# Performance work log

Measured on AMD Instinct MI355X. Metric: run time of the kernel, lower is better.

## Reference

```python
import jax, jax.numpy as jnp
import numpy as np


def _conv3x3(x, w, b):
    # standard 3x3 conv, stride 1, padding 1 (NCHW / OIHW)
    y = jax.lax.conv_general_dilated(x, w, window_strides=(1, 1),
                                     padding=((1, 1), (1, 1)),
                                     dimension_numbers=('NCHW', 'OIHW', 'NCHW'))
    return y + b[None, :, None, None]


def _bilinear_gather(img, py, px):
    # img [B,C,H,W]; py/px [B,K,H,W] fractional sample coords; zero outside (torchvision semantics)
    B, C, H, W = img.shape
    K = py.shape[1]
    y0f = jnp.floor(py)
    x0f = jnp.floor(px)
    dy = py - y0f
    dx = px - x0f
    y0 = y0f.astype(jnp.int32)
    x0 = x0f.astype(jnp.int32)
    img_f = img.reshape(B, C, H * W)

    def corner(yy, xx, wgt):
        valid = (yy >= 0) & (yy < H) & (xx >= 0) & (xx < W)
        idx = (jnp.clip(yy, 0, H - 1) * W + jnp.clip(xx, 0, W - 1)).reshape(B, -1)
        g = jax.vmap(lambda im, ix: im[:, ix])(img_f, idx)  # [B, C, K*H*W]
        return g * (wgt * valid).reshape(B, 1, -1)

    out = (corner(y0, x0, (1 - dy) * (1 - dx)) + corner(y0, x0 + 1, (1 - dy) * dx)
           + corner(y0 + 1, x0, dy * (1 - dx)) + corner(y0 + 1, x0 + 1, dy * dx))
    return out.reshape(B, C, K, H, W)


def _deform_conv(x, offset, w, b):
    # torchvision DeformConv2d, kernel 3, stride 1, pad 1, no groups
    # offset [B, 2*K, H, W], channel pairs (2k, 2k+1) = (dy, dx) for tap k
    B, C, H, W = x.shape
    K = 9
    off = offset.reshape(B, K, 2, H, W)
    ki, kj = jnp.meshgrid(jnp.arange(3), jnp.arange(3), indexing='ij')
    ki = (ki.reshape(K) - 1).astype(x.dtype)
    kj = (kj.reshape(K) - 1).astype(x.dtype)
    py = jnp.arange(H, dtype=x.dtype)[None, None, :, None] + ki[None, :, None, None] + off[:, :, 0]
    px = jnp.arange(W, dtype=x.dtype)[None, None, None, :] + kj[None, :, None, None] + off[:, :, 1]
    patches = _bilinear_gather(x, py, px)  # [B, C, K, H, W]
    out = jnp.einsum('bckhw,ock->bohw', patches, w.reshape(w.shape[0], C, K))
    return out + b[None, :, None, None]


def _maxpool2(x):
    return jax.lax.reduce_window(x, -jnp.inf, jax.lax.max, (1, 1, 2, 2), (1, 1, 2, 2), 'VALID')


def _forward(x, w_off1, b_off1, w1, b1, w_off2, b_off2, w2, b2,
             w_off3, b_off3, w3, b3, w_fc, b_fc):
    off = _conv3x3(x, w_off1, b_off1)
    h = jax.nn.relu(_deform_conv(x, off, w1, b1))
    h = _maxpool2(h)                       # [B,16,48,48]
    off = _conv3x3(h, w_off2, b_off2)
    h = jax.nn.relu(_deform_conv(h, off, w2, b2))
    h = _maxpool2(h)                       # [B,32,24,24]
    off = _conv3x3(h, w_off3, b_off3)
    h = jax.nn.relu(_deform_conv(h, off, w3, b3))  # [B,64,24,24]
    B, C, H, W = h.shape
    # adaptive avg pool to (3,3): 24 -> 3 exact bins of 8
    h = h.reshape(B, C, 3, H // 3, 3, W // 3).mean(axis=(3, 5))
    h = h.reshape(B, -1)                   # [B, 576]
    return h @ w_fc.T + b_fc


def setup_inputs() -> dict:
    key = jax.random.key(0)
    ks = jax.random.split(key, 16)
    f32 = jnp.float32

    def rn(k, shape, scale):
        return jax.random.normal(k, shape, dtype=f32) * scale

    return {
        'x': rn(ks[0], (64, 1, 96, 96), 1.0),
        # offset convs: small weights so offsets start near zero (standard deform init)
        'w_off1': rn(ks[1], (18, 1, 3, 3), 0.01), 'b_off1': jnp.zeros((18,), f32),
        'w1': rn(ks[2], (16, 1, 3, 3), 1.0 / 3.0), 'b1': jnp.zeros((16,), f32),
        'w_off2': rn(ks[3], (18, 16, 3, 3), 0.01), 'b_off2': jnp.zeros((18,), f32),
        'w2': rn(ks[4], (32, 16, 3, 3), 1.0 / 12.0), 'b2': jnp.zeros((32,), f32),
        'w_off3': rn(ks[5], (18, 32, 3, 3), 0.01), 'b_off3': jnp.zeros((18,), f32),
        'w3': rn(ks[6], (64, 32, 3, 3), 1.0 / 17.0), 'b3': jnp.zeros((64,), f32),
        'w_fc': rn(ks[7], (10, 576), 1.0 / 24.0), 'b_fc': jnp.zeros((10,), f32),
    }


def reference(x, w_off1, b_off1, w1, b1, w_off2, b_off2, w2, b2,
              w_off3, b_off3, w3, b3, w_fc, b_fc):
    return _forward(x, w_off1, b_off1, w1, b1, w_off2, b_off2, w2, b2,
                    w_off3, b_off3, w3, b3, w_fc, b_fc)
```

## Files before the change

kernel.cpp:

```cpp
#include <hip/hip_runtime.h>
#include <math.h>


template <int CIN, int COUT>
__global__ void wtrans(const float* __restrict__ w, float* __restrict__ wT) {
  int t = blockIdx.x * 256 + threadIdx.x;
  if (t >= 9 * CIN * COUT) return;
  int k = t / (CIN * COUT);
  int r = t % (CIN * COUT);
  int c = r / COUT;
  int o = r % COUT;
  wT[t] = w[(o * CIN + c) * 9 + k];
}

__global__ void deform1_fused(const float* __restrict__ x,
                              const float* __restrict__ woff,
                              const float* __restrict__ boff,
                              const float* __restrict__ w1,
                              const float* __restrict__ b1,
                              float* __restrict__ out) {
  const int H = 96, W = 96, HW = H * W;
  __shared__ float wos[9 * 18];
  __shared__ __align__(16) float ws1[9 * 16];
  for (int t = threadIdx.x; t < 9 * 18; t += 256) { int k = t / 18, tc = t % 18; wos[t] = woff[tc * 9 + k]; }
  for (int t = threadIdx.x; t < 9 * 16; t += 256) { int k = t / 16, o = t % 16; ws1[t] = w1[o * 9 + k]; }
  __syncthreads();

  int gid = blockIdx.x * 256 + threadIdx.x;
  int p2 = gid % (HW / 2);
  int b  = gid / (HW / 2);
  int xi0 = (2 * p2) % W, yi = (2 * p2) / W;
  const float* xb = x + (size_t)b * HW;

  float v[3][4];
#pragma unroll
  for (int r = 0; r < 3; ++r) {
    int yy = yi + r - 1;
    float my = (yy >= 0 && yy < H) ? 1.f : 0.f;
    int cy = min(max(yy, 0), H - 1);
#pragma unroll
    for (int c = 0; c < 4; ++c) {
      int xx = xi0 + c - 1;
      float mx = (xx >= 0 && xx < W) ? 1.f : 0.f;
      int cx = min(max(xx, 0), W - 1);
      v[r][c] = xb[cy * W + cx] * (my * mx);
    }
  }

  float off0[18], off1[18];
#pragma unroll
  for (int tc = 0; tc < 18; ++tc) { float bb = boff[tc]; off0[tc] = bb; off1[tc] = bb; }
#pragma unroll
  for (int r = 0; r < 3; ++r)
#pragma unroll
    for (int c = 0; c < 3; ++c) {
      float t0 = v[r][c], t1 = v[r][c + 1];
      const float2* wv = (const float2*)&wos[(r * 3 + c) * 18];
#pragma unroll
      for (int tt = 0; tt < 9; ++tt) {
        float2 ww = wv[tt];
        off0[2 * tt]     = fmaf(ww.x, t0, off0[2 * tt]);
        off0[2 * tt + 1] = fmaf(ww.y, t0, off0[2 * tt + 1]);
        off1[2 * tt]     = fmaf(ww.x, t1, off1[2 * tt]);
        off1[2 * tt + 1] = fmaf(ww.y, t1, off1[2 * tt + 1]);
      }
    }

  float acc0[16], acc1[16];
#pragma unroll
  for (int o = 0; o < 16; ++o) { float bb = b1[o]; acc0[o] = bb; acc1[o] = bb; }

#pragma unroll
  for (int k = 0; k < 9; ++k) {
    int dky = k / 3 - 1, dkx = k % 3 - 1;
    float val0, val1;
    {
      float py = (float)(yi + dky) + off0[2 * k];
      float px = (float)(xi0 + dkx) + off0[2 * k + 1];
      float y0f = floorf(py), x0f = floorf(px);
      float fy = py - y0f, fx = px - x0f;
      int y0 = (int)y0f, x0 = (int)x0f, y1 = y0 + 1, x1 = x0 + 1;
      float vy0 = (y0 >= 0 && y0 < H) ? 1.f : 0.f;
      float vy1 = (y1 >= 0 && y1 < H) ? 1.f : 0.f;
      float vx0 = (x0 >= 0 && x0 < W) ? 1.f : 0.f;
      float vx1 = (x1 >= 0 && x1 < W) ? 1.f : 0.f;
      float w00 = (1.f - fy) * (1.f - fx) * vy0 * vx0;
      float w01 = (1.f - fy) * fx * vy0 * vx1;
      float w10 = fy * (1.f - fx) * vy1 * vx0;
      float w11 = fy * fx * vy1 * vx1;
      int cy0 = min(max(y0, 0), H - 1), cy1 = min(max(y1, 0), H - 1);
      int cx0 = min(max(x0, 0), W - 1), cx1 = min(max(x1, 0), W - 1);
      float a = xb[cy0 * W + cx0], bb = xb[cy0 * W + cx1];
      float c = xb[cy1 * W + cx0], d = xb[cy1 * W + cx1];
      val0 = w00 * a + w01 * bb + w10 * c + w11 * d;
    }
    {
      float py = (float)(yi + dky) + off1[2 * k];
      float px = (float)(xi0 + 1 + dkx) + off1[2 * k + 1];
      float y0f = floorf(py), x0f = floorf(px);
      float fy = py - y0f, fx = px - x0f;
      int y0 = (int)y0f, x0 = (int)x0f, y1 = y0 + 1, x1 = x0 + 1;
      float vy0 = (y0 >= 0 && y0 < H) ? 1.f : 0.f;
      float vy1 = (y1 >= 0 && y1 < H) ? 1.f : 0.f;
      float vx0 = (x0 >= 0 && x0 < W) ? 1.f : 0.f;
      float vx1 = (x1 >= 0 && x1 < W) ? 1.f : 0.f;
      float w00 = (1.f - fy) * (1.f - fx) * vy0 * vx0;
      float w01 = (1.f - fy) * fx * vy0 * vx1;
      float w10 = fy * (1.f - fx) * vy1 * vx0;
      float w11 = fy * fx * vy1 * vx1;
      int cy0 = min(max(y0, 0), H - 1), cy1 = min(max(y1, 0), H - 1);
      int cx0 = min(max(x0, 0), W - 1), cx1 = min(max(x1, 0), W - 1);
      float a = xb[cy0 * W + cx0], bb = xb[cy0 * W + cx1];
      float c = xb[cy1 * W + cx0], d = xb[cy1 * W + cx1];
      val1 = w00 * a + w01 * bb + w10 * c + w11 * d;
    }
    const float4* wv = (const float4*)&ws1[k * 16];
#pragma unroll
    for (int q = 0; q < 4; ++q) {
      float4 w4 = wv[q];
      acc0[4 * q + 0] = fmaf(w4.x, val0, acc0[4 * q + 0]);
      acc0[4 * q + 1] = fmaf(w4.y, val0, acc0[4 * q + 1]);
      acc0[4 * q + 2] = fmaf(w4.z, val0, acc0[4 * q + 2]);
      acc0[4 * q + 3] = fmaf(w4.w, val0, acc0[4 * q + 3]);
      acc1[4 * q + 0] = fmaf(w4.x, val1, acc1[4 * q + 0]);
      acc1[4 * q + 1] = fmaf(w4.y, val1, acc1[4 * q + 1]);
      acc1[4 * q + 2] = fmaf(w4.z, val1, acc1[4 * q + 2]);
      acc1[4 * q + 3] = fmaf(w4.w, val1, acc1[4 * q + 3]);
    }
  }

  float* op = out + (size_t)b * 16 * HW + (size_t)yi * W + xi0;
#pragma unroll
  for (int o = 0; o < 16; ++o) {
    float2 r = make_float2(fmaxf(acc0[o], 0.f), fmaxf(acc1[o], 0.f));
    *(float2*)(op + (size_t)o * HW) = r;
  }
}

template <int C, int HI>
__global__ void pool_nchw_to_nhwc(const float* __restrict__ in,
                                  float* __restrict__ out) {
  const int HO = HI / 2, C4 = C / 4;
  int gid = blockIdx.x * blockDim.x + threadIdx.x;
  if (gid >= 64 * HO * HO * C4) return;
  int c4 = gid % C4;
  int t = gid / C4;
  int x = t % HO; t /= HO;
  int y = t % HO;
  int b = t / HO;
  float4 r;
  float* rp = &r.x;
#pragma unroll
  for (int cc = 0; cc < 4; ++cc) {
    int c = c4 * 4 + cc;
    const float* p = in + ((size_t)(b * C + c) * HI + 2 * y) * HI + 2 * x;
    rp[cc] = fmaxf(fmaxf(p[0], p[1]), fmaxf(p[HI], p[HI + 1]));
  }
  *(float4*)(out + (((size_t)b * HO + y) * HO + x) * C + c4 * 4) = r;
}

template <int CIN, int COUT, int NSPLIT>
__global__ __launch_bounds__(256, 4)
void conv3x3_off(const float* __restrict__ in,
                 const float* __restrict__ w,
                 const float* __restrict__ bias,
                 float* __restrict__ out,
                 int B, int H, int W) {
  constexpr int OC = COUT / NSPLIT;
  __shared__ float ws[9 * CIN * OC];
  int obase = blockIdx.y * OC;
  for (int t = threadIdx.x; t < 9 * CIN * OC; t += 256) {
    int k = t / (CIN * OC); int r = t % (CIN * OC);
    int c = r / OC; int o = r % OC;
    ws[t] = w[((obase + o) * CIN + c) * 9 + k];
  }
  __syncthreads();

  int gid = blockIdx.x * 256 + threadIdx.x;
  if (gid >= B * H * W) return;
  int x = gid % W; int t0 = gid / W; int y = t0 % H; int b = t0 / H;
  int HW = H * W;
  const float* inb = in + (size_t)b * HW * CIN;

  float acc[OC];
#pragma unroll
  for (int o = 0; o < OC; ++o) acc[o] = bias[obase + o];

#pragma unroll
  for (int ky = 0; ky < 3; ++ky) {
    int yy = y + ky - 1;
    if (yy < 0 || yy >= H) continue;
#pragma unroll
    for (int kx = 0; kx < 3; ++kx) {
      int xx = x + kx - 1;
      if (xx < 0 || xx >= W) continue;
      const float4* p4 = (const float4*)(inb + ((size_t)yy * W + xx) * CIN);
      int k = ky * 3 + kx;
#pragma unroll
      for (int c4 = 0; c4 < CIN / 4; ++c4) {
        float4 p = p4[c4];
        const float* pv = &p.x;
#pragma unroll
        for (int cc = 0; cc < 4; ++cc) {
          const float* wrow = &ws[(k * CIN + 4 * c4 + cc) * OC];
#pragma unroll
          for (int o = 0; o < OC; ++o) acc[o] = fmaf(wrow[o], pv[cc], acc[o]);
        }
      }
    }
  }

  float* op = out + (size_t)gid * 20 + obase;
#pragma unroll
  for (int o = 0; o < OC; ++o) op[o] = acc[o];
}

template <int CIN, int COUT, int HW_>
__global__ void deform_sgpr(const float* __restrict__ in,
                            const float* __restrict__ off_in,
                            const float* __restrict__ wT,
                            const float* __restrict__ bias,
                            float* __restrict__ out) {
  constexpr int H = HW_, W = HW_, HW = H * W;
  constexpr int PX = 64;
  constexpr int QT = CIN / 4;
  constexpr int QPT = QT / 4;
  constexpr int PSTR = 9 * CIN + 4;
  constexpr int OPG = COUT / 4;

  __shared__ __align__(16) float offs[PX * 20];
  __shared__ __align__(16) float patch[PX * PSTR];

  const int pixbase = blockIdx.x * PX;
  const int b = pixbase / HW;
  const int p0 = pixbase - b * HW;
  const float* inb = in + (size_t)b * HW * CIN;

  {
    const float4* src = (const float4*)(off_in + (size_t)pixbase * 20);
    for (int t = threadIdx.x; t < PX * 20 / 4; t += 256)
      ((float4*)offs)[t] = src[t];
  }
  __syncthreads();

  {
    int px = threadIdx.x & 63;
    int qp = threadIdx.x >> 6;
    int pib = p0 + px;
    int yi = pib / W, xi = pib % W;
#pragma unroll
    for (int k = 0; k < 9; ++k) {
      float py  = (float)(yi + k / 3 - 1) + offs[px * 20 + 2 * k];
      float pxx = (float)(xi + k % 3 - 1) + offs[px * 20 + 2 * k + 1];
      float y0f = floorf(py), x0f = floorf(pxx);
      float fy = py - y0f, fx = pxx - x0f;
      int y0 = (int)y0f, x0 = (int)x0f, y1 = y0 + 1, x1 = x0 + 1;
      float vy0 = (y0 >= 0 && y0 < H) ? 1.f : 0.f;
      float vy1 = (y1 >= 0 && y1 < H) ? 1.f : 0.f;
      float vx0 = (x0 >= 0 && x0 < W) ? 1.f : 0.f;
      float vx1 = (x1 >= 0 && x1 < W) ? 1.f : 0.f;
      float w00 = (1.f - fy) * (1.f - fx) * vy0 * vx0;
      float w01 = (1.f - fy) * fx * vy0 * vx1;
      float w10 = fy * (1.f - fx) * vy1 * vx0;
      float w11 = fy * fx * vy1 * vx1;
      int cy0 = min(max(y0, 0), H - 1), cy1 = min(max(y1, 0), H - 1);
      int cx0 = min(max(x0, 0), W - 1), cx1 = min(max(x1, 0), W - 1);
      const float* r00 = inb + ((size_t)cy0 * W + cx0) * CIN;
      const float* r01 = inb + ((size_t)cy0 * W + cx1) * CIN;
      const float* r10 = inb + ((size_t)cy1 * W + cx0) * CIN;
      const float* r11 = inb + ((size_t)cy1 * W + cx1) * CIN;
#pragma unroll
      for (int j = 0; j < QPT; ++j) {
        int q = qp + j * 4;
        float4 A  = *(const float4*)(r00 + 4 * q);
        float4 Bv = *(const float4*)(r01 + 4 * q);
        float4 Cv = *(const float4*)(r10 + 4 * q);
        float4 Dv = *(const float4*)(r11 + 4 * q);
        float4 val;
        val.x = w00 * A.x + w01 * Bv.x + w10 * Cv.x + w11 * Dv.x;
        val.y = w00 * A.y + w01 * Bv.y + w10 * Cv.y + w11 * Dv.y;
        val.z = w00 * A.z + w01 * Bv.z + w10 * Cv.z + w11 * Dv.z;
        val.w = w00 * A.w + w01 * Bv.w + w10 * Cv.w + w11 * Dv.w;
        *(float4*)&patch[px * PSTR + k * CIN + 4 * q] = val;
      }
    }
  }
  __syncthreads();

  int px = threadIdx.x & 63;
  int og = __builtin_amdgcn_readfirstlane(threadIdx.x >> 6);
  int obase = og * OPG;

  float acc[OPG];
#pragma unroll
  for (int o = 0; o < OPG; ++o) acc[o] = bias[obase + o];

  const float* patp = &patch[px * PSTR];
  for (int k = 0; k < 9; ++k) {
#pragma unroll
    for (int c4 = 0; c4 < QT; ++c4) {
      float4 p = *(const float4*)&patp[k * CIN + 4 * c4];
      const float* pv = &p.x;
      const float* wb = wT + ((size_t)(k * CIN + 4 * c4)) * COUT + obase;
#pragma unroll
      for (int cc = 0; cc < 4; ++cc)
#pragma unroll
        for (int o = 0; o < OPG; ++o)
          acc[o] = fmaf(wb[cc * COUT + o], pv[cc], acc[o]);
    }
  }

  float* ob = out + ((size_t)b * COUT + obase) * HW + p0 + px;
#pragma unroll
  for (int o = 0; o < OPG; ++o)
    ob[(size_t)o * HW] = fmaxf(acc[o], 0.f);
}

__global__ void poolfc_kernel(const float* __restrict__ h,
                              const float* __restrict__ wfc,
                              const float* __restrict__ bfc,
                              float* __restrict__ out) {
  __shared__ float feat[576];
  int b = blockIdx.x;
  int f = threadIdx.x;
  int c = f / 9, ij = f % 9, i = ij / 3, j = ij % 3;
  const float* p = h + ((size_t)(b * 64 + c) * 24 + i * 8) * 24 + j * 8;
  float s = 0.f;
#pragma unroll
  for (int r = 0; r < 8; ++r)
#pragma unroll
    for (int q = 0; q < 8; ++q)
      s += p[r * 24 + q];
  feat[f] = s * (1.f / 64.f);
  __syncthreads();
  if (f < 10) {
    float acc = bfc[f];
    const float* wp = wfc + f * 576;
    for (int t = 0; t < 576; ++t) acc = fmaf(wp[t], feat[t], acc);
    out[b * 10 + f] = acc;
  }
}

extern "C" void kernel_launch(void* const* d_in, const int* in_sizes, int n_in,
                              void* d_out, int out_size, void* d_ws, size_t ws_size,
                              hipStream_t stream) {
  const float* x      = (const float*)d_in[0];
  const float* w_off1 = (const float*)d_in[1];
  const float* b_off1 = (const float*)d_in[2];
  const float* w1     = (const float*)d_in[3];
  const float* b1     = (const float*)d_in[4];
  const float* w_off2 = (const float*)d_in[5];
  const float* b_off2 = (const float*)d_in[6];
  const float* w2     = (const float*)d_in[7];
  const float* b2     = (const float*)d_in[8];
  const float* w_off3 = (const float*)d_in[9];
  const float* b_off3 = (const float*)d_in[10];
  const float* w3     = (const float*)d_in[11];
  const float* b3     = (const float*)d_in[12];
  const float* w_fc   = (const float*)d_in[13];
  const float* b_fc   = (const float*)d_in[14];
  float* out = (float*)d_out;

  char* ws = (char*)d_ws;
  float* A   = (float*)(ws);
  float* Cp  = (float*)(ws + 18874368);
  float* Bp  = (float*)(ws + 37748736);
  float* wT2 = (float*)(ws + 47185920);
  float* wT3 = (float*)(ws + 47185920 + 9 * 16 * 32 * 4);

  const int thr = 256;

  wtrans<16, 32><<<(9 * 16 * 32 + 255) / 256, thr, 0, stream>>>(w2, wT2);
  wtrans<32, 64><<<(9 * 32 * 64 + 255) / 256, thr, 0, stream>>>(w3, wT3);

  deform1_fused<<<64 * 96 * 96 / 2 / thr, thr, 0, stream>>>(x, w_off1, b_off1, w1, b1, A);
  {
    int total = 64 * 48 * 48 * 4;
    pool_nchw_to_nhwc<16, 96><<<(total + thr - 1) / thr, thr, 0, stream>>>(A, Bp);
  }

  conv3x3_off<16, 18, 1><<<dim3(576, 1), thr, 0, stream>>>(Bp, w_off2, b_off2, Cp, 64, 48, 48);
  deform_sgpr<16, 32, 48><<<64 * 48 * 48 / 64, thr, 0, stream>>>(Bp, Cp, wT2, b2, A);
  {
    int total = 64 * 24 * 24 * 8;
    pool_nchw_to_nhwc<32, 48><<<(total + thr - 1) / thr, thr, 0, stream>>>(A, Bp);
  }

  conv3x3_off<32, 18, 3><<<dim3(144, 3), thr, 0, stream>>>(Bp, w_off3, b_off3, Cp, 64, 24, 24);
  deform_sgpr<32, 64, 24><<<64 * 24 * 24 / 64, thr, 0, stream>>>(Bp, Cp, wT3, b3, A);

  poolfc_kernel<<<64, 576, 0, stream>>>(A, w_fc, b_fc, out);
}
```

Before: 213.5 us.

## Stage deform conv weights in LDS and compute two pixels per thread

The deformable conv kernels now copy transposed weights into shared memory in tap chunks instead of reading them through wave-uniform scalar loads from global memory. Each thread computes two pixels for a narrower group of output channels, so one float4 weight load feeds both pixels' FMAs. This is meant to cut weight-load traffic and raise FMA density. In exchange it uses a lot more LDS (up to about 41KB for layer 3), which can lower occupancy, and it adds extra barriers per chunk.

```diff
diff --git a/kernel.cpp b/kernel.cpp
--- a/kernel.cpp
+++ b/kernel.cpp
@@ -215,21 +215,23 @@
   for (int o = 0; o < OC; ++o) op[o] = acc[o];
 }
 
-template <int CIN, int COUT, int HW_>
-__global__ void deform_sgpr(const float* __restrict__ in,
-                            const float* __restrict__ off_in,
-                            const float* __restrict__ wT,
-                            const float* __restrict__ bias,
-                            float* __restrict__ out) {
+template <int CIN, int COUT, int HW_, int KCHUNK>
+__global__ void deform_pre(const float* __restrict__ in,
+                           const float* __restrict__ off_in,
+                           const float* __restrict__ wT,
+                           const float* __restrict__ bias,
+                           float* __restrict__ out) {
   constexpr int H = HW_, W = HW_, HW = H * W;
   constexpr int PX = 64;
   constexpr int QT = CIN / 4;
   constexpr int QPT = QT / 4;
   constexpr int PSTR = 9 * CIN + 4;
-  constexpr int OPG = COUT / 4;
+  constexpr int OPG = COUT / 8;
+  constexpr int PP = 32;
 
   __shared__ __align__(16) float offs[PX * 20];
   __shared__ __align__(16) float patch[PX * PSTR];
+  __shared__ __align__(16) float wlds[KCHUNK * CIN * COUT];
 
   const int pixbase = blockIdx.x * PX;
   const int b = pixbase / HW;
@@ -285,35 +287,62 @@
       }
     }
   }
-  __syncthreads();
-
-  int px = threadIdx.x & 63;
-  int og = __builtin_amdgcn_readfirstlane(threadIdx.x >> 6);
+
+  int pairIdx = threadIdx.x % PP;
+  int og = threadIdx.x / PP;
   int obase = og * OPG;
-
-  float acc[OPG];
-#pragma unroll
-  for (int o = 0; o < OPG; ++o) acc[o] = bias[obase + o];
-
-  const float* patp = &patch[px * PSTR];
-  for (int k = 0; k < 9; ++k) {
-#pragma unroll
-    for (int c4 = 0; c4 < QT; ++c4) {
-      float4 p = *(const float4*)&patp[k * CIN + 4 * c4];
-      const float* pv = &p.x;
-      const float* wb = wT + ((size_t)(k * CIN + 4 * c4)) * COUT + obase;
-#pragma unroll
-      for (int cc = 0; cc < 4; ++cc)
-#pragma unroll
-        for (int o = 0; o < OPG; ++o)
-          acc[o] = fmaf(wb[cc * COUT + o], pv[cc], acc[o]);
-    }
-  }
-
-  float* ob = out + ((size_t)b * COUT + obase) * HW + p0 + px;
-#pragma unroll
-  for (int o = 0; o < OPG; ++o)
-    ob[(size_t)o * HW] = fmaxf(acc[o], 0.f);
+  int px0 = pairIdx, px1 = pairIdx + PP;
+
+  float acc0[OPG], acc1[OPG];
+#pragma unroll
+  for (int o = 0; o < OPG; ++o) { float bb = bias[obase + o]; acc0[o] = bb; acc1[o] = bb; }
+
+  const float* patp0 = &patch[px0 * PSTR];
+  const float* patp1 = &patch[px1 * PSTR];
+
+  for (int kc = 0; kc < 9; kc += KCHUNK) {
+    const int KC = (kc + KCHUNK <= 9) ? KCHUNK : (9 - kc);
+    __syncthreads();
+    {
+      const float4* src = (const float4*)(wT + (size_t)kc * CIN * COUT);
+      for (int t = threadIdx.x; t < KC * CIN * COUT / 4; t += 256)
+        ((float4*)wlds)[t] = src[t];
+    }
+    __syncthreads();
+    for (int kk = 0; kk < KC; ++kk) {
+      int k = kc + kk;
+#pragma unroll
+      for (int c4 = 0; c4 < QT; ++c4) {
+        float4 pA = *(const float4*)&patp0[k * CIN + 4 * c4];
+        float4 pB = *(const float4*)&patp1[k * CIN + 4 * c4];
+        const float* pv0 = &pA.x;
+        const float* pv1 = &pB.x;
+#pragma unroll
+        for (int cc = 0; cc < 4; ++cc) {
+          const float* wb = &wlds[((kk * CIN + 4 * c4 + cc)) * COUT + obase];
+#pragma unroll
+          for (int j = 0; j < OPG / 4; ++j) {
+            float4 wv = *(const float4*)(wb + 4 * j);
+            acc0[4 * j + 0] = fmaf(wv.x, pv0[cc], acc0[4 * j + 0]);
+            acc0[4 * j + 1] = fmaf(wv.y, pv0[cc], acc0[4 * j + 1]);
+            acc0[4 * j + 2] = fmaf(wv.z, pv0[cc], acc0[4 * j + 2]);
+            acc0[4 * j + 3] = fmaf(wv.w, pv0[cc], acc0[4 * j + 3]);
+            acc1[4 * j + 0] = fmaf(wv.x, pv1[cc], acc1[4 * j + 0]);
+            acc1[4 * j + 1] = fmaf(wv.y, pv1[cc], acc1[4 * j + 1]);
+            acc1[4 * j + 2] = fmaf(wv.z, pv1[cc], acc1[4 * j + 2]);
+            acc1[4 * j + 3] = fmaf(wv.w, pv1[cc], acc1[4 * j + 3]);
+          }
+        }
+      }
+    }
+  }
+
+  float* ob = out + ((size_t)b * COUT + obase) * HW + p0;
+#pragma unroll
+  for (int o = 0; o < OPG; ++o) {
+    ob[(size_t)o * HW + px0] = fmaxf(acc0[o], 0.f);
+    ob[(size_t)o * HW + px1] = fmaxf(acc1[o], 0.f);
+  }
 }
 
 __global__ void poolfc_kernel(const float* __restrict__ h,
@@ -380,14 +409,14 @@
   }
 
   conv3x3_off<16, 18, 1><<<dim3(576, 1), thr, 0, stream>>>(Bp, w_off2, b_off2, Cp, 64, 48, 48);
-  deform_sgpr<16, 32, 48><<<64 * 48 * 48 / 64, thr, 0, stream>>>(Bp, Cp, wT2, b2, A);
+  deform_pre<16, 32, 48, 9><<<64 * 48 * 48 / 64, thr, 0, stream>>>(Bp, Cp, wT2, b2, A);
   {
     int total = 64 * 24 * 24 * 8;
     pool_nchw_to_nhwc<32, 48><<<(total + thr - 1) / thr, thr, 0, stream>>>(A, Bp);
   }
 
   conv3x3_off<32, 18, 3><<<dim3(144, 3), thr, 0, stream>>>(Bp, w_off3, b_off3, Cp, 64, 24, 24);
-  deform_sgpr<32, 64, 24><<<64 * 24 * 24 / 64, thr, 0, stream>>>(Bp, Cp, wT3, b3, A);
+  deform_pre<32, 64, 24, 5><<<64 * 24 * 24 / 64, thr, 0, stream>>>(Bp, Cp, wT3, b3, A);
 
   poolfc_kernel<<<64, 576, 0, stream>>>(A, w_fc, b_fc, out);
 }
```

After: 226.3 us. 6.0% more time.
